# Optimization experiments

Hardware: AMD Instinct MI355X
Metric: run time of the kernel (lower is better)

The kernel has to match this reference:

```python
import jax, jax.numpy as jnp
import numpy as np

FEATURES = 4
HIDDEN = 32


def setup_inputs() -> dict:
    key = jax.random.key(0)
    ks = jax.random.split(key, 12)
    n_nodes, n_edges = 100000, 2500000
    x = jax.random.normal(ks[0], (n_nodes, FEATURES), dtype=jnp.float32)
    edge_index = jax.random.randint(ks[1], (2, n_edges), 0, n_nodes, dtype=jnp.int64)
    def glorot(k, fan_in, fan_out):
        s = jnp.sqrt(6.0 / (fan_in + fan_out)).astype(jnp.float32)
        return jax.random.uniform(k, (fan_in, fan_out), jnp.float32, -s, s)
    return {
        "x": x,
        "edge_index": edge_index,
        "W1": glorot(ks[2], FEATURES, HIDDEN), "b1": jnp.zeros((HIDDEN,), jnp.float32),
        "W2": glorot(ks[3], HIDDEN, HIDDEN),   "b2": jnp.zeros((HIDDEN,), jnp.float32),
        "W21": glorot(ks[4], HIDDEN, HIDDEN),  "b21": jnp.zeros((HIDDEN,), jnp.float32),
        "W3": glorot(ks[5], HIDDEN, 1),        "b3": jnp.zeros((1,), jnp.float32),
    }


def _gcn_norm(edge_index, n_nodes):
    # Add self-loops, compute symmetric normalization deg^-1/2[dst]*deg^-1/2[src]
    loops = jnp.arange(n_nodes, dtype=edge_index.dtype)
    src = jnp.concatenate([edge_index[0], loops])
    dst = jnp.concatenate([edge_index[1], loops])
    deg = jax.ops.segment_sum(jnp.ones_like(dst, dtype=jnp.float32), dst, num_segments=n_nodes)
    dinv = jnp.where(deg > 0, jax.lax.rsqrt(deg), 0.0)
    norm = dinv[src] * dinv[dst]  # [E+N]
    return src, dst, norm


def _gcn_layer(x, W, b, src, dst, norm, n_nodes):
    h = x @ W                                   # [N, out]
    msg = h[src] * norm[:, None]                # gather + scale
    out = jax.ops.segment_sum(msg, dst, num_segments=n_nodes)  # scatter-add
    return out + b


def reference(x, edge_index, W1, b1, W2, b2, W21, b21, W3, b3):
    n_nodes = x.shape[0]
    src, dst, norm = _gcn_norm(edge_index, n_nodes)
    h = jax.nn.relu(_gcn_layer(x, W1, b1, src, dst, norm, n_nodes))
    h = jax.nn.relu(_gcn_layer(h, W2, b2, src, dst, norm, n_nodes))
    h = jax.nn.relu(_gcn_layer(h, W21, b21, src, dst, norm, n_nodes))
    return _gcn_layer(h, W3, b3, src, dst, norm, n_nodes)
```

## Files before the change

### kernel.cpp

```cpp
#include <hip/hip_runtime.h>
#include <hip/hip_fp16.h>

#define FEATS 4
#define HID 32
#define BLK 256
#define CAP 64
#define PW 256
#define PSHIFT 8
#define PCAP 8192
#define NPB 512
#define PBLK 1024
#define MAXK 8
#define MAXNP 512

static inline int cdiv(long long a, int b) { return (int)((a + b - 1) / b); }

struct __align__(8) half4v { __half2 a, b; };

__global__ void k_zero_i(int* __restrict__ p, int n) {
    int i = blockIdx.x * blockDim.x + threadIdx.x;
    if (i < n) p[i] = 0;
}

__global__ void __launch_bounds__(PBLK, 4)
k_partition(const int* __restrict__ src, const int* __restrict__ dst,
            int* __restrict__ part_fill, unsigned int* __restrict__ part_edges,
            int e, int np) {
    __shared__ int lcnt[MAXNP];
    __shared__ int lbase[MAXNP];
    for (int p = threadIdx.x; p < np; p += blockDim.x) lcnt[p] = 0;
    __syncthreads();
    int chunk = (e + gridDim.x - 1) / gridDim.x;
    int lo = blockIdx.x * chunk;
    int hi = min(lo + chunk, e);
    unsigned pw[MAXK];
    int pp[MAXK];
#pragma unroll
    for (int k = 0; k < MAXK; k++) {
        int j = lo + threadIdx.x + k * (int)blockDim.x;
        if (j < hi) {
            int d = dst[j], s = src[j];
            int p = d >> PSHIFT;
            pp[k] = p;
            pw[k] = (unsigned)s | ((unsigned)(d & (PW - 1)) << 24);
            atomicAdd(&lcnt[p], 1);
        } else pp[k] = -1;
    }
    __syncthreads();
    for (int p = threadIdx.x; p < np; p += blockDim.x) {
        int c = lcnt[p];
        lbase[p] = c ? atomicAdd(&part_fill[p], c) : 0;
        lcnt[p] = 0;
    }
    __syncthreads();
#pragma unroll
    for (int k = 0; k < MAXK; k++) {
        if (pp[k] >= 0) {
            int p = pp[k];
            int pos = lbase[p] + atomicAdd(&lcnt[p], 1);
            if (pos < PCAP) part_edges[(size_t)p * PCAP + pos] = pw[k];
        }
    }
}

__global__ void k_local_csr(const int* __restrict__ part_fill,
                            const unsigned int* __restrict__ part_edges,
                            const float4* __restrict__ x,
                            int* __restrict__ cnt_g, float* __restrict__ dinv,
                            float4* __restrict__ xn, int* __restrict__ bucket, int n) {
    __shared__ int cnt[PW];
    int p = blockIdx.x;
    if (threadIdx.x < PW) cnt[threadIdx.x] = 0;
    __syncthreads();
    int m = min(part_fill[p], PCAP);
    const unsigned int* pe = part_edges + (size_t)p * PCAP;
    int base_node = p << PSHIFT;
    for (int j = threadIdx.x; j < m; j += blockDim.x) {
        unsigned v = pe[j];
        int local = (int)(v >> 24);
        int s = (int)(v & 0xFFFFFFu);
        int pos = atomicAdd(&cnt[local], 1);
        if (pos < CAP) bucket[(size_t)(base_node + local) * CAP + pos] = s;
    }
    __syncthreads();
    if (threadIdx.x < PW) {
        int node = base_node + threadIdx.x;
        if (node < n) {
            int dg = cnt[threadIdx.x];
            cnt_g[node] = dg;
            float s = rsqrtf((float)(dg + 1));
            dinv[node] = s;
            float4 v = x[node];
            v.x *= s; v.y *= s; v.z *= s; v.w *= s;
            xn[node] = v;
        }
    }
}

__global__ void k_dinv(const int* __restrict__ deg, float* __restrict__ dinv, int n) {
    int i = blockIdx.x * blockDim.x + threadIdx.x;
    if (i < n) dinv[i] = rsqrtf((float)(deg[i] + 1));
}

__global__ void k_gather4_f12(const int* __restrict__ cnt, const int* __restrict__ bucket,
                              const float4* __restrict__ xn, const float* __restrict__ dinv,
                              const float* __restrict__ W1, const float* __restrict__ b1,
                              const float* __restrict__ W2, float* __restrict__ hn, int n) {
    __shared__ float4 sW1[FEATS * 8];
    __shared__ float4 sB1[8];
    __shared__ float4 sW2[HID * 8];
    int tid = threadIdx.x;
    if (tid < FEATS * 8) sW1[tid] = ((const float4*)W1)[tid];
    if (tid < 8) sB1[tid] = ((const float4*)b1)[tid];
    sW2[tid] = ((const float4*)W2)[tid];
    __syncthreads();
    int gid = blockIdx.x * blockDim.x + tid;
    int node = gid >> 3;
    int cq = gid & 7;
    if (node >= n) return;
    int dg = min(cnt[node], CAP);
    const int* row = bucket + (size_t)node * CAP;
    float4 acc = make_float4(0.f, 0.f, 0.f, 0.f);
    int j = cq;
    for (; j + 8 < dg; j += 16) {
        int s0 = row[j], s1 = row[j + 8];
        float4 v0 = xn[s0];
        float4 v1 = xn[s1];
        acc.x += v0.x + v1.x; acc.y += v0.y + v1.y;
        acc.z += v0.z + v1.z; acc.w += v0.w + v1.w;
    }
    if (j < dg) {
        float4 v = xn[row[j]];
        acc.x += v.x; acc.y += v.y; acc.z += v.z; acc.w += v.w;
    }
#pragma unroll
    for (int m = 1; m < 8; m <<= 1) {
        acc.x += __shfl_xor(acc.x, m, 8);
        acc.y += __shfl_xor(acc.y, m, 8);
        acc.z += __shfl_xor(acc.z, m, 8);
        acc.w += __shfl_xor(acc.w, m, 8);
    }
    float sc = dinv[node];
    float4 self = xn[node];
    float4 a;
    a.x = sc * (acc.x + self.x);
    a.y = sc * (acc.y + self.y);
    a.z = sc * (acc.z + self.z);
    a.w = sc * (acc.w + self.w);
    float4 w0 = sW1[0 * 8 + cq], w1 = sW1[1 * 8 + cq];
    float4 w2 = sW1[2 * 8 + cq], w3 = sW1[3 * 8 + cq];
    float4 y = sB1[cq];
    y.x += a.x * w0.x + a.y * w1.x + a.z * w2.x + a.w * w3.x;
    y.y += a.x * w0.y + a.y * w1.y + a.z * w2.y + a.w * w3.y;
    y.z += a.x * w0.z + a.y * w1.z + a.z * w2.z + a.w * w3.z;
    y.w += a.x * w0.w + a.y * w1.w + a.z * w2.w + a.w * w3.w;
    y.x = fmaxf(y.x, 0.f); y.y = fmaxf(y.y, 0.f);
    y.z = fmaxf(y.z, 0.f); y.w = fmaxf(y.w, 0.f);
    float4 o = make_float4(0.f, 0.f, 0.f, 0.f);
#pragma unroll
    for (int r = 0; r < 8; r++) {
        float4 v;
        v.x = __shfl(y.x, r, 8);
        v.y = __shfl(y.y, r, 8);
        v.z = __shfl(y.z, r, 8);
        v.w = __shfl(y.w, r, 8);
        float4 wa = sW2[(4 * r + 0) * 8 + cq];
        float4 wb = sW2[(4 * r + 1) * 8 + cq];
        float4 wc = sW2[(4 * r + 2) * 8 + cq];
        float4 wd = sW2[(4 * r + 3) * 8 + cq];
        o.x += v.x * wa.x + v.y * wb.x + v.z * wc.x + v.w * wd.x;
        o.y += v.x * wa.y + v.y * wb.y + v.z * wc.y + v.w * wd.y;
        o.z += v.x * wa.z + v.y * wb.z + v.z * wc.z + v.w * wd.z;
        o.w += v.x * wa.w + v.y * wb.w + v.z * wc.w + v.w * wd.w;
    }
    o.x *= sc; o.y *= sc; o.z *= sc; o.w *= sc;
    half4v st;
    st.a = __floats2half2_rn(o.x, o.y);
    st.b = __floats2half2_rn(o.z, o.w);
    ((half4v*)hn)[node * 8 + cq] = st;
}

template <int K, int C>
__global__ void k_mm(const float* __restrict__ in, const float* __restrict__ W,
                     const float* __restrict__ dinv, float* __restrict__ hn, int n) {
    __shared__ float sW[K * C];
    for (int i = threadIdx.x; i < K * C; i += blockDim.x) sW[i] = W[i];
    __syncthreads();
    int gid = blockIdx.x * blockDim.x + threadIdx.x;
    int node = gid / C, c = gid % C;
    if (node >= n) return;
    float acc = 0.0f;
#pragma unroll
    for (int k = 0; k < K; k++) acc += in[node * K + k] * sW[k * C + c];
    hn[node * C + c] = acc * dinv[node];
}

#define ACC4(v) do { acc.x += (v).x; acc.y += (v).y; acc.z += (v).z; acc.w += (v).w; } while (0)

#define ACCH(v) do {                                                         \
        float2 f0 = __half22float2((v).a);                                   \
        float2 f1 = __half22float2((v).b);                                   \
        acc.x += f0.x; acc.y += f0.y; acc.z += f1.x; acc.w += f1.y;          \
    } while (0)

#define GATHER_BODY_H()                                                      \
    int dg = min(cnt[node], CAP);                                            \
    const half4v* hp = (const half4v*)hn;                                    \
    const int* row = bucket + (size_t)node * CAP;                            \
    float4 acc;                                                              \
    {                                                                        \
        half4v hs = hp[node * 8 + cq];                                       \
        float2 f0 = __half22float2(hs.a);                                    \
        float2 f1 = __half22float2(hs.b);                                    \
        acc = make_float4(f0.x, f0.y, f1.x, f1.y);                           \
    }                                                                        \
    int j = 0;                                                               \
    for (; j + 8 <= dg; j += 8) {                                            \
        int4 sa = *(const int4*)(row + j);                                   \
        int4 sb = *(const int4*)(row + j + 4);                               \
        half4v v0 = hp[sa.x * 8 + cq];                                       \
        half4v v1 = hp[sa.y * 8 + cq];                                       \
        half4v v2 = hp[sa.z * 8 + cq];                                       \
        half4v v3 = hp[sa.w * 8 + cq];                                       \
        half4v v4 = hp[sb.x * 8 + cq];                                       \
        half4v v5 = hp[sb.y * 8 + cq];                                       \
        half4v v6 = hp[sb.z * 8 + cq];                                       \
        half4v v7 = hp[sb.w * 8 + cq];                                       \
        ACCH(v0); ACCH(v1); ACCH(v2); ACCH(v3);                              \
        ACCH(v4); ACCH(v5); ACCH(v6); ACCH(v7);                              \
    }                                                                        \
    if (j + 4 <= dg) {                                                       \
        int4 s4 = *(const int4*)(row + j);                                   \
        half4v v0 = hp[s4.x * 8 + cq];                                       \
        half4v v1 = hp[s4.y * 8 + cq];                                       \
        half4v v2 = hp[s4.z * 8 + cq];                                       \
        half4v v3 = hp[s4.w * 8 + cq];                                       \
        ACCH(v0); ACCH(v1); ACCH(v2); ACCH(v3);                              \
        j += 4;                                                              \
    }                                                                        \
    for (; j < dg; j++) {                                                    \
        half4v v = hp[row[j] * 8 + cq];                                      \
        ACCH(v);                                                             \
    }

__global__ void k_gather_fmm(const int* __restrict__ cnt, const int* __restrict__ bucket,
                             const float* __restrict__ hn, const float* __restrict__ dinv,
                             const float* __restrict__ bias, const float* __restrict__ Wn,
                             float* __restrict__ hn3, int n) {
    __shared__ float4 sW[HID * 8];
    sW[threadIdx.x] = ((const float4*)Wn)[threadIdx.x];
    __syncthreads();
    int gid = blockIdx.x * blockDim.x + threadIdx.x;
    int node = gid >> 3;
    int cq = gid & 7;
    if (node >= n) return;
    GATHER_BODY_H()
    float sc = dinv[node];
    float4 b = ((const float4*)bias)[cq];
    float4 y;
    y.x = fmaxf(sc * acc.x + b.x, 0.f);
    y.y = fmaxf(sc * acc.y + b.y, 0.f);
    y.z = fmaxf(sc * acc.z + b.z, 0.f);
    y.w = fmaxf(sc * acc.w + b.w, 0.f);
    float4 o = make_float4(0.f, 0.f, 0.f, 0.f);
#pragma unroll
    for (int r = 0; r < 8; r++) {
        float4 v;
        v.x = __shfl(y.x, r, 8);
        v.y = __shfl(y.y, r, 8);
        v.z = __shfl(y.z, r, 8);
        v.w = __shfl(y.w, r, 8);
        float4 w0 = sW[(4 * r + 0) * 8 + cq];
        float4 w1 = sW[(4 * r + 1) * 8 + cq];
        float4 w2 = sW[(4 * r + 2) * 8 + cq];
        float4 w3 = sW[(4 * r + 3) * 8 + cq];
        o.x += v.x * w0.x + v.y * w1.x + v.z * w2.x + v.w * w3.x;
        o.y += v.x * w0.y + v.y * w1.y + v.z * w2.y + v.w * w3.y;
        o.z += v.x * w0.z + v.y * w1.z + v.z * w2.z + v.w * w3.z;
        o.w += v.x * w0.w + v.y * w1.w + v.z * w2.w + v.w * w3.w;
    }
    o.x *= sc; o.y *= sc; o.z *= sc; o.w *= sc;
    half4v st;
    st.a = __floats2half2_rn(o.x, o.y);
    st.b = __floats2half2_rn(o.z, o.w);
    ((half4v*)hn3)[node * 8 + cq] = st;
}

__global__ void k_gather_fdot(const int* __restrict__ cnt, const int* __restrict__ bucket,
                              const float* __restrict__ hn, const float* __restrict__ dinv,
                              const float* __restrict__ bias, const float* __restrict__ W3,
                              float* __restrict__ hn4, int n) {
    int gid = blockIdx.x * blockDim.x + threadIdx.x;
    int node = gid >> 3;
    int cq = gid & 7;
    if (node >= n) return;
    GATHER_BODY_H()
    float sc = dinv[node];
    float4 b = ((const float4*)bias)[cq];
    float4 w = ((const float4*)W3)[cq];
    float p = fmaxf(sc * acc.x + b.x, 0.f) * w.x
            + fmaxf(sc * acc.y + b.y, 0.f) * w.y
            + fmaxf(sc * acc.z + b.z, 0.f) * w.z
            + fmaxf(sc * acc.w + b.w, 0.f) * w.w;
#pragma unroll
    for (int o = 4; o > 0; o >>= 1) p += __shfl_down(p, o, 8);
    if (cq == 0) hn4[node] = p * sc;
}

__global__ void k_gather1b(const int* __restrict__ cnt, const int* __restrict__ bucket,
                           const float* __restrict__ hn, const float* __restrict__ dinv,
                           const float* __restrict__ b, float* __restrict__ out, int n) {
    int gid = blockIdx.x * blockDim.x + threadIdx.x;
    int node = gid >> 3;
    int lane = gid & 7;
    if (node >= n) return;
    int dg = min(cnt[node], CAP);
    const int* row = bucket + (size_t)node * CAP;
    float acc = (lane == 0) ? hn[node] : 0.0f;
    int j = lane;
    for (; j + 8 < dg; j += 16) {
        float a0 = hn[row[j]];
        float a1 = hn[row[j + 8]];
        acc += a0 + a1;
    }
    if (j < dg) acc += hn[row[j]];
#pragma unroll
    for (int o = 4; o > 0; o >>= 1) acc += __shfl_down(acc, o, 8);
    if (lane == 0) out[node] = dinv[node] * acc + b[0];
}

__global__ void k_deg_count(const int* __restrict__ dst, int* __restrict__ deg, int e) {
    int i = blockIdx.x * blockDim.x + threadIdx.x;
    if (i < e) atomicAdd(&deg[dst[i]], 1);
}

__global__ void k_block_scan(const int* __restrict__ deg, int* __restrict__ exc,
                             int* __restrict__ blk_sums, int n) {
    __shared__ int s[BLK];
    int i = blockIdx.x * BLK + threadIdx.x;
    int v = (i < n) ? deg[i] : 0;
    s[threadIdx.x] = v;
    __syncthreads();
    for (int off = 1; off < BLK; off <<= 1) {
        int t = (threadIdx.x >= (unsigned)off) ? s[threadIdx.x - off] : 0;
        __syncthreads();
        s[threadIdx.x] += t;
        __syncthreads();
    }
    if (i < n) exc[i] = s[threadIdx.x] - v;
    if (threadIdx.x == BLK - 1) blk_sums[blockIdx.x] = s[threadIdx.x];
}

__global__ void k_scan_sums(int* __restrict__ blk_sums, int nb) {
    __shared__ int s[1024];
    __shared__ int carry;
    if (threadIdx.x == 0) carry = 0;
    __syncthreads();
    for (int base = 0; base < nb; base += 1024) {
        int i = base + threadIdx.x;
        int v = (i < nb) ? blk_sums[i] : 0;
        s[threadIdx.x] = v;
        __syncthreads();
        for (int off = 1; off < 1024; off <<= 1) {
            int t = (threadIdx.x >= (unsigned)off) ? s[threadIdx.x - off] : 0;
            __syncthreads();
            s[threadIdx.x] += t;
            __syncthreads();
        }
        if (i < nb) blk_sums[i] = s[threadIdx.x] - v + carry;
        __syncthreads();
        if (threadIdx.x == 0) carry += s[1023];
        __syncthreads();
    }
}

__global__ void k_add_off(const int* __restrict__ exc, const int* __restrict__ blk_sums,
                          int* __restrict__ row_start, int* __restrict__ fill, int n) {
    int i = blockIdx.x * blockDim.x + threadIdx.x;
    if (i < n) {
        int rs = exc[i] + blk_sums[i / BLK];
        row_start[i] = rs;
        fill[i] = rs;
    }
}

__global__ void k_scatter(const int* __restrict__ src, const int* __restrict__ dst,
                          int* __restrict__ fill, int* __restrict__ csr_src, int e) {
    int i = blockIdx.x * blockDim.x + threadIdx.x;
    if (i < e) {
        int pos = atomicAdd(&fill[dst[i]], 1);
        csr_src[pos] = src[i];
    }
}

template <bool RELU>
__global__ void k_gather32(const int* __restrict__ row_start, const int* __restrict__ deg,
                           const int* __restrict__ csr_src, const float* __restrict__ hn,
                           const float* __restrict__ dinv, const float* __restrict__ bias,
                           float* __restrict__ y, int n) {
    int gid = blockIdx.x * blockDim.x + threadIdx.x;
    int node = gid >> 3;
    int cq = gid & 7;
    if (node >= n) return;
    int rs = row_start[node], dg = deg[node];
    const float4* hp = (const float4*)hn;
    float4 acc = hp[node * 8 + cq];
    for (int j = 0; j < dg; j++) {
        int s = csr_src[rs + j];
        float4 v = hp[s * 8 + cq];
        ACC4(v);
    }
    float sc = dinv[node];
    float4 b = ((const float4*)bias)[cq];
    float4 r;
    r.x = sc * acc.x + b.x; r.y = sc * acc.y + b.y;
    r.z = sc * acc.z + b.z; r.w = sc * acc.w + b.w;
    if (RELU) {
        r.x = fmaxf(r.x, 0.0f); r.y = fmaxf(r.y, 0.0f);
        r.z = fmaxf(r.z, 0.0f); r.w = fmaxf(r.w, 0.0f);
    }
    ((float4*)y)[node * 8 + cq] = r;
}

__global__ void k_gather1(const int* __restrict__ row_start, const int* __restrict__ deg,
                          const int* __restrict__ csr_src, const float* __restrict__ hn,
                          const float* __restrict__ dinv, const float* __restrict__ b,
                          float* __restrict__ out, int n) {
    int gid = blockIdx.x * blockDim.x + threadIdx.x;
    int node = gid >> 3;
    int lane = gid & 7;
    if (node >= n) return;
    int rs = row_start[node], dg = deg[node];
    float acc = (lane == 0) ? hn[node] : 0.0f;
    for (int j = lane; j < dg; j += 8) acc += hn[csr_src[rs + j]];
#pragma unroll
    for (int o = 4; o > 0; o >>= 1) acc += __shfl_down(acc, o, 8);
    if (lane == 0) out[node] = dinv[node] * acc + b[0];
}

extern "C" void kernel_launch(void* const* d_in, const int* in_sizes, int n_in,
                              void* d_out, int out_size, void* d_ws, size_t ws_size,
                              hipStream_t stream) {
    const float* x   = (const float*)d_in[0];
    const int*   ei  = (const int*)d_in[1];
    const float* W1  = (const float*)d_in[2];
    const float* b1  = (const float*)d_in[3];
    const float* W2  = (const float*)d_in[4];
    const float* b2  = (const float*)d_in[5];
    const float* W21 = (const float*)d_in[6];
    const float* b21 = (const float*)d_in[7];
    const float* W3  = (const float*)d_in[8];
    const float* b3  = (const float*)d_in[9];
    float* out = (float*)d_out;

    const int n = in_sizes[0] / FEATS;
    const int e = in_sizes[1] / 2;
    const int* src = ei;
    const int* dst = ei + e;
    const int nb = cdiv(n, BLK);
    const int np = cdiv(n, PW);

    auto align256 = [](size_t v) { return (v + 255) & ~(size_t)255; };
    const long long n8 = (long long)n * 8;

    size_t sz_cnt    = align256((size_t)n * 4);
    size_t sz_dinv   = align256((size_t)n * 4);
    size_t sz_f4     = align256((size_t)n * 16);
    size_t sz_bucket = align256((size_t)n * CAP * 4);
    size_t sz_hn     = align256((size_t)n * HID * 4);
    size_t sz_part   = align256((size_t)np * PCAP * 4) + align256((size_t)np * 4);
    size_t region    = 2 * sz_hn > sz_part ? 2 * sz_hn : sz_part;
    size_t need = sz_cnt + sz_dinv + sz_f4 + sz_bucket + region;

    if (ws_size >= need && np <= MAXNP && (long long)e <= (long long)NPB * PBLK * MAXK) {
        char* ws = (char*)d_ws;
        size_t off = 0;
        int*    cnt_g  = (int*)(ws + off);    off += sz_cnt;
        float*  dinv   = (float*)(ws + off);  off += sz_dinv;
        float4* xn     = (float4*)(ws + off); off += sz_f4;
        int*    bucket = (int*)(ws + off);    off += sz_bucket;
        char*   reg    = ws + off;
        float* hn = (float*)reg;
        float* yb = (float*)(reg + sz_hn);
        unsigned int* part_edges = (unsigned int*)reg;
        int* part_fill = (int*)(reg + align256((size_t)np * PCAP * 4));

        k_zero_i<<<cdiv(np, BLK), BLK, 0, stream>>>(part_fill, np);
        k_partition<<<NPB, PBLK, 0, stream>>>(src, dst, part_fill, part_edges, e, np);
        k_local_csr<<<np, PBLK, 0, stream>>>(part_fill, part_edges, (const float4*)x,
                                             cnt_g, dinv, xn, bucket, n);

        k_gather4_f12<<<cdiv(n8, BLK), BLK, 0, stream>>>(cnt_g, bucket, xn, dinv,
                                                         W1, b1, W2, hn, n);

        k_gather_fmm<<<cdiv(n8, BLK), BLK, 0, stream>>>(cnt_g, bucket, hn, dinv, b2, W21, yb, n);
        k_gather_fdot<<<cdiv(n8, BLK), BLK, 0, stream>>>(cnt_g, bucket, yb, dinv, b21, W3, hn, n);
        k_gather1b<<<cdiv(n8, BLK), BLK, 0, stream>>>(cnt_g, bucket, hn, dinv, b3, out, n);
    } else {
        const long long nc = (long long)n * HID;
        char* ws = (char*)d_ws;
        size_t off = 0;
        int*   deg_i     = (int*)(ws + off);   off += align256((size_t)n * 4);
        int*   exc       = (int*)(ws + off);   off += align256((size_t)n * 4);
        int*   row_start = (int*)(ws + off);   off += align256((size_t)n * 4);
        int*   fill      = (int*)(ws + off);   off += align256((size_t)n * 4);
        int*   blk_sums  = (int*)(ws + off);   off += align256((size_t)nb * 4);
        float* dinv      = (float*)(ws + off); off += align256((size_t)n * 4);
        int*   csr_src   = (int*)(ws + off);   off += align256((size_t)e * 4);
        float* hn        = (float*)(ws + off); off += align256((size_t)n * HID * 4);
        float* yb        = (float*)(ws + off); off += align256((size_t)n * HID * 4);

        k_zero_i<<<nb, BLK, 0, stream>>>(deg_i, n);
        k_deg_count<<<cdiv(e, BLK), BLK, 0, stream>>>(dst, deg_i, e);
        k_dinv<<<nb, BLK, 0, stream>>>(deg_i, dinv, n);
        k_block_scan<<<nb, BLK, 0, stream>>>(deg_i, exc, blk_sums, n);
        k_scan_sums<<<1, 1024, 0, stream>>>(blk_sums, nb);
        k_add_off<<<nb, BLK, 0, stream>>>(exc, blk_sums, row_start, fill, n);
        k_scatter<<<cdiv(e, BLK), BLK, 0, stream>>>(src, dst, fill, csr_src, e);

        k_mm<FEATS, HID><<<cdiv(nc, BLK), BLK, 0, stream>>>(x, W1, dinv, hn, n);
        k_gather32<true><<<cdiv(n8, BLK), BLK, 0, stream>>>(row_start, deg_i, csr_src, hn, dinv, b1, yb, n);

        k_mm<HID, HID><<<cdiv(nc, BLK), BLK, 0, stream>>>(yb, W2, dinv, hn, n);
        k_gather32<true><<<cdiv(n8, BLK), BLK, 0, stream>>>(row_start, deg_i, csr_src, hn, dinv, b2, yb, n);

        k_mm<HID, HID><<<cdiv(nc, BLK), BLK, 0, stream>>>(yb, W21, dinv, hn, n);
        k_gather32<true><<<cdiv(n8, BLK), BLK, 0, stream>>>(row_start, deg_i, csr_src, hn, dinv, b21, yb, n);

        k_mm<HID, 1><<<cdiv(n, BLK), BLK, 0, stream>>>(yb, W3, dinv, hn, n);
        k_gather1<<<cdiv(n8, BLK), BLK, 0, stream>>>(row_start, deg_i, csr_src, hn, dinv, b3, out, n);
    }
}
```

Measured before the change: 225.0 us.

## Sort nodes by in-degree to balance gather work; use nontemporal index loads

Builds a degree histogram in the local CSR kernel, scans it, and computes a permutation that groups nodes by in-degree bucket. The four gather kernels then process nodes in permuted order, so lanes and wavefronts handle similar-degree nodes and divergence is reduced. Bucket index loads also become nontemporal to reduce cache pollution. This adds two small kernels plus a perm read per node, and it loses the natural sequential node ordering, so output writes and self-feature reads become scattered.

```diff
diff --git a/kernel.cpp b/kernel.cpp
--- a/kernel.cpp
+++ b/kernel.cpp
@@ -17,6 +17,8 @@
 
 struct __align__(8) half4v { __half2 a, b; };
 
+typedef int vint4 __attribute__((ext_vector_type(4)));
+
 __global__ void k_zero_i(int* __restrict__ p, int n) {
     int i = blockIdx.x * blockDim.x + threadIdx.x;
     if (i < n) p[i] = 0;
@@ -67,10 +69,13 @@
                             const unsigned int* __restrict__ part_edges,
                             const float4* __restrict__ x,
                             int* __restrict__ cnt_g, float* __restrict__ dinv,
-                            float4* __restrict__ xn, int* __restrict__ bucket, int n) {
+                            float4* __restrict__ xn, int* __restrict__ bucket,
+                            int* __restrict__ hist, int n) {
     __shared__ int cnt[PW];
+    __shared__ int lh[64];
     int p = blockIdx.x;
     if (threadIdx.x < PW) cnt[threadIdx.x] = 0;
+    if (threadIdx.x < 64) lh[threadIdx.x] = 0;
     __syncthreads();
     int m = min(part_fill[p], PCAP);
     const unsigned int* pe = part_edges + (size_t)p * PCAP;
@@ -93,7 +98,46 @@
             float4 v = x[node];
             v.x *= s; v.y *= s; v.z *= s; v.w *= s;
             xn[node] = v;
+            atomicAdd(&lh[min(dg, 63)], 1);
         }
+    }
+    __syncthreads();
+    if (threadIdx.x < 64) {
+        int c = lh[threadIdx.x];
+        if (c) atomicAdd(&hist[threadIdx.x], c);
+    }
+}
+
+__global__ void k_scan64(const int* __restrict__ hist, int* __restrict__ base) {
+    if (threadIdx.x == 0) {
+        int s = 0;
+        for (int i = 0; i < 64; i++) { base[i] = s; s += hist[i]; }
+    }
+}
+
+__global__ void __launch_bounds__(1024)
+k_perm(const int* __restrict__ cnt, int* __restrict__ base,
+       int* __restrict__ perm, int n) {
+    __shared__ int lh[64];
+    __shared__ int lb[64];
+    int chunk = (n + gridDim.x - 1) / gridDim.x;
+    int lo = blockIdx.x * chunk;
+    int hi = min(lo + chunk, n);
+    if (threadIdx.x < 64) lh[threadIdx.x] = 0;
+    __syncthreads();
+    for (int i = lo + threadIdx.x; i < hi; i += 1024)
+        atomicAdd(&lh[min(cnt[i], 63)], 1);
+    __syncthreads();
+    if (threadIdx.x < 64) {
+        int c = lh[threadIdx.x];
+        lb[threadIdx.x] = c ? atomicAdd(&base[threadIdx.x], c) : 0;
+        lh[threadIdx.x] = 0;
+    }
+    __syncthreads();
+    for (int i = lo + threadIdx.x; i < hi; i += 1024) {
+        int b = min(cnt[i], 63);
+        int off = atomicAdd(&lh[b], 1);
+        perm[lb[b] + off] = i;
     }
 }
 
@@ -102,7 +146,8 @@
     if (i < n) dinv[i] = rsqrtf((float)(deg[i] + 1));
 }
 
-__global__ void k_gather4_f12(const int* __restrict__ cnt, const int* __restrict__ bucket,
+__global__ void k_gather4_f12(const int* __restrict__ perm, const int* __restrict__ cnt,
+                              const int* __restrict__ bucket,
                               const float4* __restrict__ xn, const float* __restrict__ dinv,
                               const float* __restrict__ W1, const float* __restrict__ b1,
                               const float* __restrict__ W2, float* __restrict__ hn, int n) {
@@ -115,22 +160,24 @@
     sW2[tid] = ((const float4*)W2)[tid];
     __syncthreads();
     int gid = blockIdx.x * blockDim.x + tid;
-    int node = gid >> 3;
+    int nodeIdx = gid >> 3;
     int cq = gid & 7;
-    if (node >= n) return;
+    if (nodeIdx >= n) return;
+    int node = perm[nodeIdx];
     int dg = min(cnt[node], CAP);
     const int* row = bucket + (size_t)node * CAP;
     float4 acc = make_float4(0.f, 0.f, 0.f, 0.f);
     int j = cq;
     for (; j + 8 < dg; j += 16) {
-        int s0 = row[j], s1 = row[j + 8];
+        int s0 = __builtin_nontemporal_load(row + j);
+        int s1 = __builtin_nontemporal_load(row + j + 8);
         float4 v0 = xn[s0];
         float4 v1 = xn[s1];
         acc.x += v0.x + v1.x; acc.y += v0.y + v1.y;
         acc.z += v0.z + v1.z; acc.w += v0.w + v1.w;
     }
     if (j < dg) {
-        float4 v = xn[row[j]];
+        float4 v = xn[__builtin_nontemporal_load(row + j)];
         acc.x += v.x; acc.y += v.y; acc.z += v.z; acc.w += v.w;
     }
 #pragma unroll
@@ -216,8 +263,8 @@
     }                                                                        \
     int j = 0;                                                               \
     for (; j + 8 <= dg; j += 8) {                                            \
-        int4 sa = *(const int4*)(row + j);                                   \
-        int4 sb = *(const int4*)(row + j + 4);                               \
+        vint4 sa = __builtin_nontemporal_load((const vint4*)(row + j));      \
+        vint4 sb = __builtin_nontemporal_load((const vint4*)(row + j + 4));  \
         half4v v0 = hp[sa.x * 8 + cq];                                       \
         half4v v1 = hp[sa.y * 8 + cq];                                       \
         half4v v2 = hp[sa.z * 8 + cq];                                       \
@@ -230,7 +277,7 @@
         ACCH(v4); ACCH(v5); ACCH(v6); ACCH(v7);                              \
     }                                                                        \
     if (j + 4 <= dg) {                                                       \
-        int4 s4 = *(const int4*)(row + j);                                   \
+        vint4 s4 = __builtin_nontemporal_load((const vint4*)(row + j));      \
         half4v v0 = hp[s4.x * 8 + cq];                                       \
         half4v v1 = hp[s4.y * 8 + cq];                                       \
         half4v v2 = hp[s4.z * 8 + cq];                                       \
@@ -243,7 +290,8 @@
         ACCH(v);                                                             \
     }
 
-__global__ void k_gather_fmm(const int* __restrict__ cnt, const int* __restrict__ bucket,
+__global__ void k_gather_fmm(const int* __restrict__ perm, const int* __restrict__ cnt,
+                             const int* __restrict__ bucket,
                              const float* __restrict__ hn, const float* __restrict__ dinv,
                              const float* __restrict__ bias, const float* __restrict__ Wn,
                              float* __restrict__ hn3, int n) {
@@ -251,9 +299,10 @@
     sW[threadIdx.x] = ((const float4*)Wn)[threadIdx.x];
     __syncthreads();
     int gid = blockIdx.x * blockDim.x + threadIdx.x;
-    int node = gid >> 3;
+    int nodeIdx = gid >> 3;
     int cq = gid & 7;
-    if (node >= n) return;
+    if (nodeIdx >= n) return;
+    int node = perm[nodeIdx];
     GATHER_BODY_H()
     float sc = dinv[node];
     float4 b = ((const float4*)bias)[cq];
@@ -286,14 +335,16 @@
     ((half4v*)hn3)[node * 8 + cq] = st;
 }
 
-__global__ void k_gather_fdot(const int* __restrict__ cnt, const int* __restrict__ bucket,
+__global__ void k_gather_fdot(const int* __restrict__ perm, const int* __restrict__ cnt,
+                              const int* __restrict__ bucket,
                               const float* __restrict__ hn, const float* __restrict__ dinv,
                               const float* __restrict__ bias, const float* __restrict__ W3,
                               float* __restrict__ hn4, int n) {
     int gid = blockIdx.x * blockDim.x + threadIdx.x;
-    int node = gid >> 3;
+    int nodeIdx = gid >> 3;
     int cq = gid & 7;
-    if (node >= n) return;
+    if (nodeIdx >= n) return;
+    int node = perm[nodeIdx];
     GATHER_BODY_H()
     float sc = dinv[node];
     float4 b = ((const float4*)bias)[cq];
@@ -307,23 +358,25 @@
     if (cq == 0) hn4[node] = p * sc;
 }
 
-__global__ void k_gather1b(const int* __restrict__ cnt, const int* __restrict__ bucket,
+__global__ void k_gather1b(const int* __restrict__ perm, const int* __restrict__ cnt,
+                           const int* __restrict__ bucket,
                            const float* __restrict__ hn, const float* __restrict__ dinv,
                            const float* __restrict__ b, float* __restrict__ out, int n) {
     int gid = blockIdx.x * blockDim.x + threadIdx.x;
-    int node = gid >> 3;
+    int nodeIdx = gid >> 3;
     int lane = gid & 7;
-    if (node >= n) return;
+    if (nodeIdx >= n) return;
+    int node = perm[nodeIdx];
     int dg = min(cnt[node], CAP);
     const int* row = bucket + (size_t)node * CAP;
     float acc = (lane == 0) ? hn[node] : 0.0f;
     int j = lane;
     for (; j + 8 < dg; j += 16) {
-        float a0 = hn[row[j]];
-        float a1 = hn[row[j + 8]];
+        float a0 = hn[__builtin_nontemporal_load(row + j)];
+        float a1 = hn[__builtin_nontemporal_load(row + j + 8)];
         acc += a0 + a1;
     }
-    if (j < dg) acc += hn[row[j]];
+    if (j < dg) acc += hn[__builtin_nontemporal_load(row + j)];
 #pragma unroll
     for (int o = 4; o > 0; o >>= 1) acc += __shfl_down(acc, o, 8);
     if (lane == 0) out[node] = dinv[node] * acc + b[0];
@@ -467,10 +520,11 @@
     size_t sz_dinv   = align256((size_t)n * 4);
     size_t sz_f4     = align256((size_t)n * 16);
     size_t sz_bucket = align256((size_t)n * CAP * 4);
+    size_t sz_perm   = align256((size_t)n * 4);
     size_t sz_hn     = align256((size_t)n * HID * 4);
-    size_t sz_part   = align256((size_t)np * PCAP * 4) + align256((size_t)np * 4);
+    size_t sz_part   = align256((size_t)np * PCAP * 4) + align256((size_t)np * 4 + 512);
     size_t region    = 2 * sz_hn > sz_part ? 2 * sz_hn : sz_part;
-    size_t need = sz_cnt + sz_dinv + sz_f4 + sz_bucket + region;
+    size_t need = sz_cnt + sz_dinv + sz_f4 + sz_bucket + sz_perm + region;
 
     if (ws_size >= need && np <= MAXNP && (long long)e <= (long long)NPB * PBLK * MAXK) {
         char* ws = (char*)d_ws;
@@ -479,23 +533,31 @@
         float*  dinv   = (float*)(ws + off);  off += sz_dinv;
         float4* xn     = (float4*)(ws + off); off += sz_f4;
         int*    bucket = (int*)(ws + off);    off += sz_bucket;
+        int*    perm   = (int*)(ws + off);    off += sz_perm;
         char*   reg    = ws + off;
         float* hn = (float*)reg;
         float* yb = (float*)(reg + sz_hn);
         unsigned int* part_edges = (unsigned int*)reg;
         int* part_fill = (int*)(reg + align256((size_t)np * PCAP * 4));
-
-        k_zero_i<<<cdiv(np, BLK), BLK, 0, stream>>>(part_fill, np);
+        int* hist = part_fill + np;
+        int* dbase = hist + 64;
+
+        k_zero_i<<<cdiv(np + 128, BLK), BLK, 0, stream>>>(part_fill, np + 128);
         k_partition<<<NPB, PBLK, 0, stream>>>(src, dst, part_fill, part_edges, e, np);
         k_local_csr<<<np, PBLK, 0, stream>>>(part_fill, part_edges, (const float4*)x,
-                                             cnt_g, dinv, xn, bucket, n);
-
-        k_gather4_f12<<<cdiv(n8, BLK), BLK, 0, stream>>>(cnt_g, bucket, xn, dinv,
+                                             cnt_g, dinv, xn, bucket, hist, n);
+        k_scan64<<<1, 64, 0, stream>>>(hist, dbase);
+        k_perm<<<128, 1024, 0, stream>>>(cnt_g, dbase, perm, n);
+
+        k_gather4_f12<<<cdiv(n8, BLK), BLK, 0, stream>>>(perm, cnt_g, bucket, xn, dinv,
                                                          W1, b1, W2, hn, n);
 
-        k_gather_fmm<<<cdiv(n8, BLK), BLK, 0, stream>>>(cnt_g, bucket, hn, dinv, b2, W21, yb, n);
-        k_gather_fdot<<<cdiv(n8, BLK), BLK, 0, stream>>>(cnt_g, bucket, yb, dinv, b21, W3, hn, n);
-        k_gather1b<<<cdiv(n8, BLK), BLK, 0, stream>>>(cnt_g, bucket, hn, dinv, b3, out, n);
+        k_gather_fmm<<<cdiv(n8, BLK), BLK, 0, stream>>>(perm, cnt_g, bucket, hn, dinv,
+                                                        b2, W21, yb, n);
+        k_gather_fdot<<<cdiv(n8, BLK), BLK, 0, stream>>>(perm, cnt_g, bucket, yb, dinv,
+                                                         b21, W3, hn, n);
+        k_gather1b<<<cdiv(n8, BLK), BLK, 0, stream>>>(perm, cnt_g, bucket, hn, dinv,
+                                                      b3, out, n);
     } else {
         const long long nc = (long long)n * HID;
         char* ws = (char*)d_ws;
```

Measured after the change: 254.3 us. 1.13x slower.
